# Performance work log

Measured on AMD Instinct MI355X. Metric: run time of the kernel, lower is better.

## Reference

```python
import jax, jax.numpy as jnp
import numpy as np

N_NODES = 50000
N_EDGES = 800000
F_IN = 1024
F_MID = 256
DROP_P = 0.5


def gcn_conv(x, W, b, src, dst, norm, n_nodes):
    # x: [N, Fin], W: [Fin, Fout]. PyG GCNConv: out = scatter(norm * (xW)[src] -> dst) + b
    h = x @ W                                  # [N, Fout]
    msg = h[src] * norm[:, None]               # [E+N, Fout] gathered, normalized messages
    out = jax.ops.segment_sum(msg, dst, num_segments=n_nodes)
    return out + b


def setup_inputs() -> dict:
    key = jax.random.key(0)
    k1, k2, k3, k4, k5 = jax.random.split(key, 5)
    x = jax.random.normal(k1, (N_NODES, F_IN), dtype=jnp.float32)
    edge_index = jax.random.randint(k2, (2, N_EDGES), 0, N_NODES, dtype=jnp.int64)
    # Glorot-ish init for GCN weights
    W1 = jax.random.normal(k3, (F_IN, F_MID), dtype=jnp.float32) / np.sqrt(F_IN)
    b1 = jnp.zeros((F_MID,), dtype=jnp.float32)
    W2 = jax.random.normal(k4, (F_MID, F_IN), dtype=jnp.float32) / np.sqrt(F_MID)
    b2 = jnp.zeros((F_IN,), dtype=jnp.float32)
    return {"x": x, "edge_index": edge_index, "W1": W1, "b1": b1, "W2": W2, "b2": b2}


def reference(x, edge_index, W1, b1, W2, b2):
    n = x.shape[0]
    # add self-loops (PyG GCNConv default add_self_loops=True)
    loop = jnp.arange(n, dtype=edge_index.dtype)
    src = jnp.concatenate([edge_index[0], loop])
    dst = jnp.concatenate([edge_index[1], loop])
    # symmetric normalization D^-1/2 (A+I) D^-1/2
    deg = jax.ops.segment_sum(jnp.ones_like(dst, dtype=x.dtype), dst, num_segments=n)
    dinv = jnp.where(deg > 0, jax.lax.rsqrt(deg), 0.0)
    norm = dinv[src] * dinv[dst]               # [E+N]

    h = jax.nn.relu(gcn_conv(x, W1, b1, src, dst, norm, n))
    # F.dropout(x) default: p=0.5, training=True -> deterministic mask w/ fixed key
    keep = jax.random.bernoulli(jax.random.key(42), 1.0 - DROP_P, h.shape)
    h = jnp.where(keep, h / (1.0 - DROP_P), 0.0)
    out = gcn_conv(h, W2, b2, src, dst, norm, n)
    return out
```

## Files before the change

### kernel.cpp

```cpp
#include <hip/hip_runtime.h>
#include <hip/hip_bf16.h>

#define N_NODES 50000
#define N_EDGES 800000
#define F_IN 1024
#define F_MID 256

typedef _Float16 f16;
typedef _Float16 f16x4 __attribute__((ext_vector_type(4)));
typedef _Float16 f16x8 __attribute__((ext_vector_type(8)));
typedef float f32x4 __attribute__((ext_vector_type(4)));

__device__ __forceinline__ void glds16(const f16* g, f16* l) {
    __builtin_amdgcn_global_load_lds(
        (const __attribute__((address_space(1))) unsigned int*)g,
        (__attribute__((address_space(3))) unsigned int*)l, 16, 0, 0);
}

__device__ __forceinline__ void tf_round(unsigned &x0, unsigned &x1, int r) {
    x0 += x1;
    x1 = (x1 << r) | (x1 >> (32 - r));
    x1 ^= x0;
}

__device__ __forceinline__ int keep_mask(unsigned f) {
    const unsigned ks0 = 0u, ks1 = 42u;
    const unsigned ks2 = ks0 ^ ks1 ^ 0x1BD11BDAu;
    unsigned x0 = 0u + ks0;
    unsigned x1 = f + ks1;
    tf_round(x0,x1,13); tf_round(x0,x1,15); tf_round(x0,x1,26); tf_round(x0,x1,6);
    x0 += ks1; x1 += ks2 + 1u;
    tf_round(x0,x1,17); tf_round(x0,x1,29); tf_round(x0,x1,16); tf_round(x0,x1,24);
    x0 += ks2; x1 += ks0 + 2u;
    tf_round(x0,x1,13); tf_round(x0,x1,15); tf_round(x0,x1,26); tf_round(x0,x1,6);
    x0 += ks0; x1 += ks1 + 3u;
    tf_round(x0,x1,17); tf_round(x0,x1,29); tf_round(x0,x1,16); tf_round(x0,x1,24);
    x0 += ks1; x1 += ks2 + 4u;
    tf_round(x0,x1,13); tf_round(x0,x1,15); tf_round(x0,x1,26); tf_round(x0,x1,6);
    x0 += ks2; x1 += ks0 + 5u;
    return (((x0 ^ x1) >> 31) == 0u);
}

__device__ __forceinline__ int ld_src(const int* ei, int e, int is64) {
    return is64 ? ei[2 * e] : ei[e];
}
__device__ __forceinline__ int ld_dst(const int* ei, int e, int is64) {
    return is64 ? ei[2 * N_EDGES + 2 * e] : ei[N_EDGES + e];
}

__global__ __launch_bounds__(256) void k_prep(const float* __restrict__ W1, f16* __restrict__ W1T,
                                              const int* __restrict__ ei,
                                              int* deg, int* cursor, int* counter, int* flag) {
    const int tid = threadIdx.x;
    const int gid = blockIdx.x * 256 + tid;
    const int gstr = gridDim.x * 256;
    if (gid < N_NODES) { deg[gid] = 0; cursor[gid] = 0; }
    if (gid == 0) counter[0] = 0;
    if (blockIdx.x == 0) {
        if (tid == 0) flag[0] = 1;
        __syncthreads();
        int nz = 0;
        for (int k = tid; k < 1024; k += 256) nz |= (ei[2 * k + 1] != 0);
        if (nz) atomicAnd(flag, 0);
    }
    for (int i = gid; i < F_IN * F_MID; i += gstr) {
        int k = i >> 8, n = i & 255;
        W1T[(size_t)n * F_IN + (k ^ ((n & 7) << 3))] = (f16)W1[i];
    }
}

__global__ __launch_bounds__(256) void k_rows(const int* __restrict__ deg, float* __restrict__ dinv,
                                              int* __restrict__ rowst, int* __restrict__ counter) {
    int i = blockIdx.x * 256 + threadIdx.x;
    if (i < N_NODES) {
        dinv[i] = rsqrtf((float)(deg[i] + 1));
        rowst[i] = atomicAdd(counter, deg[i]);
    }
}

__global__ __launch_bounds__(256) void k_fill(const int* __restrict__ ei, const int* __restrict__ rowst,
                                              int* __restrict__ cursor, int* __restrict__ csr,
                                              const int* __restrict__ flag) {
    int e = blockIdx.x * 256 + threadIdx.x;
    int is64 = flag[0];
    if (e < N_EDGES) {
        int d = ld_dst(ei, e, is64);
        int pos = rowst[d] + atomicAdd(&cursor[d], 1);
        csr[pos] = ld_src(ei, e, is64);
    }
}

template<int BM, int BN, int TN, bool A16, bool C16>
__global__ __launch_bounds__(TN) void k_mfma(const void* __restrict__ Ag,
                                             const f16* __restrict__ BTg,
                                             void* __restrict__ Cg,
                                             const float* __restrict__ bias,
                                             int M, int Ntot, int K, int mainx,
                                             const int* __restrict__ ei, int* __restrict__ deg,
                                             const int* __restrict__ flag,
                                             const float* __restrict__ Wr, f16* __restrict__ WrT) {
    if ((int)blockIdx.x >= mainx) {
        const int str = (gridDim.x - mainx) * TN;
        const int t0 = (blockIdx.x - mainx) * TN + threadIdx.x;
        const int is64 = flag[0];
        for (int e = t0; e < N_EDGES; e += str)
            atomicAdd(&deg[ld_dst(ei, e, is64)], 1);
        for (int i = t0; i < F_MID * F_IN; i += str) {
            int k = i >> 10, n = i & 1023;
            WrT[(size_t)n * F_MID + (k ^ ((n & 7) << 3))] = (f16)Wr[i];
        }
        return;
    }

    constexpr int BK = 64;
    constexpr int NW = TN / 64;
    constexpr int WM = BM / 64;
    constexpr int WN = NW / WM;
    constexpr int WTN = BN / WN;
    constexpr int FN = WTN / 16;
    __shared__ f16 As[2][BM * BK];
    __shared__ f16 Bs[2][BN * BK];

    const int tid = threadIdx.x, lane = tid & 63, wid = tid >> 6;
    const int wm = wid % WM, wn = wid / WM;
    const int row0 = blockIdx.x * BM, col0 = blockIdx.y * BN;

    f32x4 acc[4][FN] = {};
    const int ar = tid >> 3;
    const int ac = (tid & 7) * 8;
    f32x4 av0 = {}, av1 = {};

    const int nkt = K / BK;
    int buf = 0;

    auto stage_load = [&](int kt, int b) {
        const int k0 = kt * BK;
        if constexpr (A16) {
            const f16* A = (const f16*)Ag;
            constexpr int nA = BM / 8 / NW;
            #pragma unroll
            for (int j = 0; j < nA; ++j) {
                int i = wid * nA + j;
                int li = i * 512 + lane * 8;
                int r = li >> 6, c = li & 63;
                glds16(&A[(size_t)(row0 + r) * K + k0 + c], &As[b][i * 512]);
            }
        } else {
            const float* A = (const float*)Ag;
            int gr = row0 + ar;
            if (gr < M) {
                av0 = *(const f32x4*)&A[(size_t)gr * K + k0 + ac];
                av1 = *(const f32x4*)&A[(size_t)gr * K + k0 + ac + 4];
            } else { av0 = (f32x4){}; av1 = (f32x4){}; }
        }
        constexpr int nB = BN / 8 / NW;
        #pragma unroll
        for (int j = 0; j < nB; ++j) {
            int i = wid * nB + j;
            int li = i * 512 + lane * 8;
            int r = li >> 6, c = li & 63;
            glds16(&BTg[(size_t)(col0 + r) * K + k0 + c], &Bs[b][i * 512]);
        }
    };
    auto stage_write = [&](int b) {
        if constexpr (!A16) {
            f16x4 l = __builtin_convertvector(av0, f16x4);
            f16x4 h = __builtin_convertvector(av1, f16x4);
            f16x8 v = { l[0], l[1], l[2], l[3], h[0], h[1], h[2], h[3] };
            *(f16x8*)&As[b][ar * 64 + (ac ^ ((ar & 7) << 3))] = v;
        }
    };

    stage_load(0, 0);
    stage_write(0);
    __syncthreads();

    for (int kt = 0; kt < nkt; ++kt) {
        if (kt + 1 < nkt) stage_load(kt + 1, buf ^ 1);
        #pragma unroll
        for (int ks = 0; ks < 2; ++ks) {
            const int cc = ks * 32 + (lane >> 4) * 8;
            f16x8 af[4], bf[FN];
            #pragma unroll
            for (int m = 0; m < 4; ++m) {
                int r = wm * 64 + m * 16 + (lane & 15);
                af[m] = *(const f16x8*)&As[buf][r * 64 + (cc ^ ((r & 7) << 3))];
            }
            #pragma unroll
            for (int n = 0; n < FN; ++n) {
                int r = wn * WTN + n * 16 + (lane & 15);
                bf[n] = *(const f16x8*)&Bs[buf][r * 64 + (cc ^ ((r & 7) << 3))];
            }
            #pragma unroll
            for (int m = 0; m < 4; ++m)
                #pragma unroll
                for (int n = 0; n < FN; ++n)
                    acc[m][n] = __builtin_amdgcn_mfma_f32_16x16x32_f16(af[m], bf[n], acc[m][n], 0, 0, 0);
        }
        if (kt + 1 < nkt) stage_write(buf ^ 1);
        __syncthreads();
        buf ^= 1;
    }

    const int rbase = row0 + wm * 64 + (lane >> 4) * 4;
    const int cbase = col0 + wn * WTN + (lane & 15);
    #pragma unroll
    for (int m = 0; m < 4; ++m) {
        #pragma unroll
        for (int j = 0; j < 4; ++j) {
            const int r = rbase + m * 16 + j;
            if (r >= M) continue;
            if constexpr (C16) {
                f16* C = (f16*)Cg;
                #pragma unroll
                for (int n = 0; n < FN; ++n)
                    C[(size_t)r * Ntot + cbase + n * 16] = (f16)acc[m][n][j];
            } else {
                float* C = (float*)Cg;
                #pragma unroll
                for (int n = 0; n < FN; ++n) {
                    const int c = cbase + n * 16;
                    C[(size_t)r * Ntot + c] = acc[m][n][j] + bias[c];
                }
            }
        }
    }
}

template<int POST, int SWZ, int SCALED_IN>
__global__ __launch_bounds__(256) void k_agg16(const f16* __restrict__ hin,
                                               f16* __restrict__ hout,
                                               const int* __restrict__ csr,
                                               const int* __restrict__ rowst,
                                               const int* __restrict__ deg,
                                               const float* __restrict__ dinv,
                                               const float* __restrict__ bias) {
    const int wid = threadIdx.x >> 6;
    const int lane = threadIdx.x & 63;
    const int row = blockIdx.x * 4 + wid;
    const int start = rowst[row];
    const int cnt = deg[row];
    const int ch = lane * 4;
    const float di = dinv[row];

    f32x4 acc = __builtin_convertvector(*(const f16x4*)&hin[(size_t)row * F_MID + ch], f32x4);
    if (!SCALED_IN) acc *= di;
    int k = 0;
    for (; k + 4 <= cnt; k += 4) {
        const int s0 = csr[start + k], s1 = csr[start + k + 1];
        const int s2 = csr[start + k + 2], s3 = csr[start + k + 3];
        f16x4 v0 = *(const f16x4*)&hin[(size_t)s0 * F_MID + ch];
        f16x4 v1 = *(const f16x4*)&hin[(size_t)s1 * F_MID + ch];
        f16x4 v2 = *(const f16x4*)&hin[(size_t)s2 * F_MID + ch];
        f16x4 v3 = *(const f16x4*)&hin[(size_t)s3 * F_MID + ch];
        if (SCALED_IN) {
            acc += __builtin_convertvector(v0, f32x4) + __builtin_convertvector(v1, f32x4)
                 + __builtin_convertvector(v2, f32x4) + __builtin_convertvector(v3, f32x4);
        } else {
            acc += dinv[s0] * __builtin_convertvector(v0, f32x4)
                 + dinv[s1] * __builtin_convertvector(v1, f32x4)
                 + dinv[s2] * __builtin_convertvector(v2, f32x4)
                 + dinv[s3] * __builtin_convertvector(v3, f32x4);
        }
    }
    for (; k < cnt; ++k) {
        const int s = csr[start + k];
        f32x4 v = __builtin_convertvector(*(const f16x4*)&hin[(size_t)s * F_MID + ch], f32x4);
        acc += SCALED_IN ? v : dinv[s] * v;
    }
    acc *= di;

    if (POST) {
        const unsigned f0 = (unsigned)row * F_MID + (unsigned)ch;
        #pragma unroll
        for (int j = 0; j < 4; ++j) {
            float t = acc[j] + bias[ch + j];
            t = fmaxf(t, 0.0f);
            t = keep_mask(f0 + j) ? t * 2.0f : 0.0f;
            acc[j] = t * di;
        }
    }
    const int oc = SWZ ? (ch ^ ((row & 7) << 3)) : ch;
    *(f16x4*)&hout[(size_t)row * F_MID + oc] = __builtin_convertvector(acc, f16x4);
}

extern "C" void kernel_launch(void* const* d_in, const int* in_sizes, int n_in,
                              void* d_out, int out_size, void* d_ws, size_t ws_size,
                              hipStream_t stream) {
    const float* x  = (const float*)d_in[0];
    const int*   ei = (const int*)d_in[1];
    const float* W1 = (const float*)d_in[2];
    const float* b1 = (const float*)d_in[3];
    const float* W2 = (const float*)d_in[4];
    const float* b2 = (const float*)d_in[5];
    float* out = (float*)d_out;

    f16* h0 = (f16*)out;
    f16* h1s = h0 + (size_t)N_NODES * F_MID;

    f16*   h2agg = (f16*)d_ws;
    f16*   W1T   = h2agg + (size_t)(N_NODES + 64) * F_MID;
    f16*   W2T   = W1T + (size_t)F_MID * F_IN;
    float* dinv  = (float*)(W2T + (size_t)F_IN * F_MID);
    int*   deg   = (int*)(dinv + N_NODES);
    int*   rowst = deg + N_NODES;
    int*   cursor= rowst + N_NODES;
    int*   csr   = cursor + N_NODES;
    int*   counter = csr + N_EDGES;
    int*   flag    = counter + 1;

    k_prep<<<256, 256, 0, stream>>>(W1, W1T, ei, deg, cursor, counter, flag);

    {
        const int mainx = (N_NODES + 63) / 64;
        dim3 grid(mainx + 384, 1);
        k_mfma<64, 256, 512, false, true><<<grid, 512, 0, stream>>>(
            (const void*)x, W1T, (void*)h0, nullptr, N_NODES, F_MID, F_IN,
            mainx, ei, deg, flag, W2, W2T);
    }

    k_rows<<<(N_NODES + 255) / 256, 256, 0, stream>>>(deg, dinv, rowst, counter);
    k_fill<<<(N_EDGES + 255) / 256, 256, 0, stream>>>(ei, rowst, cursor, csr, flag);

    k_agg16<1, 0, 0><<<N_NODES / 4, 256, 0, stream>>>(h0, h1s, csr, rowst, deg, dinv, b1);
    k_agg16<0, 1, 1><<<N_NODES / 4, 256, 0, stream>>>(h1s, h2agg, csr, rowst, deg, dinv, nullptr);

    {
        const int mainx = (N_NODES + 63) / 64;
        dim3 grid(mainx, 4);
        k_mfma<64, 256, 512, true, false><<<grid, 512, 0, stream>>>(
            (const void*)h2agg, W2T, (void*)out, b2, N_NODES, F_IN, F_MID,
            mainx, ei, deg, flag, W2, W2T);
    }
}
```

Measured before the change: 349.9 us.

## Stage GEMM epilogue through LDS for vectorized coalesced stores, add nontemporal loads

The MFMA GEMM epilogue now writes accumulators into a shared-memory tile, which aliases the staging buffers, and then emits 16-byte coalesced global stores. Previously it did scattered scalar stores per lane. Fp32 input loads and the final output stores become nontemporal, and the number of auxiliary prep blocks launched alongside the first GEMM drops. The aim is to cut store transaction count and cache pollution, at the cost of an extra barrier and LDS round-trip in the epilogue.

```diff
diff --git a/kernel.cpp b/kernel.cpp
--- a/kernel.cpp
+++ b/kernel.cpp
@@ -118,10 +118,16 @@
     constexpr int WN = NW / WM;
     constexpr int WTN = BN / WN;
     constexpr int FN = WTN / 16;
-    __shared__ f16 As[2][BM * BK];
-    __shared__ f16 Bs[2][BN * BK];
+    constexpr int SMEM_STG = (2 * BM * BK + 2 * BN * BK) * 2;
+    constexpr int LDC = BN + 8;
+    constexpr int SMEM_EPI = BM * LDC * (C16 ? 2 : 4);
+    constexpr int SMEM_SZ = SMEM_STG > SMEM_EPI ? SMEM_STG : SMEM_EPI;
+    __shared__ __align__(16) char smem[SMEM_SZ];
+    f16* As_ = (f16*)smem;
+    f16* Bs_ = As_ + 2 * BM * BK;
 
     const int tid = threadIdx.x, lane = tid & 63, wid = tid >> 6;
+    const int l15 = lane & 15;
     const int wm = wid % WM, wn = wid / WM;
     const int row0 = blockIdx.x * BM, col0 = blockIdx.y * BN;
 
@@ -137,29 +143,25 @@
         const int k0 = kt * BK;
         if constexpr (A16) {
             const f16* A = (const f16*)Ag;
-            constexpr int nA = BM / 8 / NW;
-            #pragma unroll
-            for (int j = 0; j < nA; ++j) {
-                int i = wid * nA + j;
+            #pragma unroll
+            for (int i = wid; i < BM * BK / 512; i += NW) {
                 int li = i * 512 + lane * 8;
                 int r = li >> 6, c = li & 63;
-                glds16(&A[(size_t)(row0 + r) * K + k0 + c], &As[b][i * 512]);
+                glds16(&A[(size_t)(row0 + r) * K + k0 + c], &As_[b * BM * BK + i * 512]);
             }
         } else {
             const float* A = (const float*)Ag;
             int gr = row0 + ar;
             if (gr < M) {
-                av0 = *(const f32x4*)&A[(size_t)gr * K + k0 + ac];
-                av1 = *(const f32x4*)&A[(size_t)gr * K + k0 + ac + 4];
+                av0 = __builtin_nontemporal_load((const f32x4*)&A[(size_t)gr * K + k0 + ac]);
+                av1 = __builtin_nontemporal_load((const f32x4*)&A[(size_t)gr * K + k0 + ac + 4]);
             } else { av0 = (f32x4){}; av1 = (f32x4){}; }
         }
-        constexpr int nB = BN / 8 / NW;
-        #pragma unroll
-        for (int j = 0; j < nB; ++j) {
-            int i = wid * nB + j;
+        #pragma unroll
+        for (int i = wid; i < BN * BK / 512; i += NW) {
             int li = i * 512 + lane * 8;
             int r = li >> 6, c = li & 63;
-            glds16(&BTg[(size_t)(col0 + r) * K + k0 + c], &Bs[b][i * 512]);
+            glds16(&BTg[(size_t)(col0 + r) * K + k0 + c], &Bs_[b * BN * BK + i * 512]);
         }
     };
     auto stage_write = [&](int b) {
@@ -167,7 +169,7 @@
             f16x4 l = __builtin_convertvector(av0, f16x4);
             f16x4 h = __builtin_convertvector(av1, f16x4);
             f16x8 v = { l[0], l[1], l[2], l[3], h[0], h[1], h[2], h[3] };
-            *(f16x8*)&As[b][ar * 64 + (ac ^ ((ar & 7) << 3))] = v;
+            *(f16x8*)&As_[b * BM * BK + ar * 64 + (ac ^ ((ar & 7) << 3))] = v;
         }
     };
 
@@ -183,13 +185,13 @@
             f16x8 af[4], bf[FN];
             #pragma unroll
             for (int m = 0; m < 4; ++m) {
-                int r = wm * 64 + m * 16 + (lane & 15);
-                af[m] = *(const f16x8*)&As[buf][r * 64 + (cc ^ ((r & 7) << 3))];
+                int r = wm * 64 + m * 16 + l15;
+                af[m] = *(const f16x8*)&As_[buf * BM * BK + r * 64 + (cc ^ ((r & 7) << 3))];
             }
             #pragma unroll
             for (int n = 0; n < FN; ++n) {
-                int r = wn * WTN + n * 16 + (lane & 15);
-                bf[n] = *(const f16x8*)&Bs[buf][r * 64 + (cc ^ ((r & 7) << 3))];
+                int r = wn * WTN + n * 16 + l15;
+                bf[n] = *(const f16x8*)&Bs_[buf * BN * BK + r * 64 + (cc ^ ((r & 7) << 3))];
             }
             #pragma unroll
             for (int m = 0; m < 4; ++m)
@@ -202,26 +204,51 @@
         buf ^= 1;
     }
 
-    const int rbase = row0 + wm * 64 + (lane >> 4) * 4;
-    const int cbase = col0 + wn * WTN + (lane & 15);
-    #pragma unroll
-    for (int m = 0; m < 4; ++m) {
-        #pragma unroll
-        for (int j = 0; j < 4; ++j) {
-            const int r = rbase + m * 16 + j;
-            if (r >= M) continue;
-            if constexpr (C16) {
-                f16* C = (f16*)Cg;
+    if constexpr (C16) {
+        f16* CT = (f16*)smem;
+        #pragma unroll
+        for (int m = 0; m < 4; ++m)
+            #pragma unroll
+            for (int j = 0; j < 4; ++j) {
+                const int rl = wm * 64 + m * 16 + (lane >> 4) * 4 + j;
                 #pragma unroll
                 for (int n = 0; n < FN; ++n)
-                    C[(size_t)r * Ntot + cbase + n * 16] = (f16)acc[m][n][j];
-            } else {
-                float* C = (float*)Cg;
+                    CT[rl * LDC + wn * WTN + n * 16 + l15] = (f16)acc[m][n][j];
+            }
+        __syncthreads();
+        f16* C = (f16*)Cg;
+        constexpr int NCH = BM * BN / 8;
+        #pragma unroll
+        for (int ci = tid; ci < NCH; ci += TN) {
+            const int r = ci / (BN / 8), c = (ci % (BN / 8)) * 8;
+            const int gr = row0 + r;
+            if (gr < M) {
+                f16x8 v = *(const f16x8*)&CT[r * LDC + c];
+                *(f16x8*)&C[(size_t)gr * Ntot + col0 + c] = v;
+            }
+        }
+    } else {
+        float* CT = (float*)smem;
+        #pragma unroll
+        for (int m = 0; m < 4; ++m)
+            #pragma unroll
+            for (int j = 0; j < 4; ++j) {
+                const int rl = wm * 64 + m * 16 + (lane >> 4) * 4 + j;
                 #pragma unroll
-                for (int n = 0; n < FN; ++n) {
-                    const int c = cbase + n * 16;
-                    C[(size_t)r * Ntot + c] = acc[m][n][j] + bias[c];
-                }
+                for (int n = 0; n < FN; ++n)
+                    CT[rl * LDC + wn * WTN + n * 16 + l15] = acc[m][n][j];
+            }
+        __syncthreads();
+        float* C = (float*)Cg;
+        constexpr int NCH = BM * BN / 4;
+        #pragma unroll
+        for (int ci = tid; ci < NCH; ci += TN) {
+            const int r = ci / (BN / 4), c = (ci % (BN / 4)) * 4;
+            const int gr = row0 + r;
+            if (gr < M) {
+                f32x4 v = *(const f32x4*)&CT[r * LDC + c];
+                v += *(const f32x4*)&bias[col0 + c];
+                __builtin_nontemporal_store(v, (f32x4*)&C[(size_t)gr * Ntot + col0 + c]);
             }
         }
     }
@@ -313,7 +340,7 @@
 
     {
         const int mainx = (N_NODES + 63) / 64;
-        dim3 grid(mainx + 384, 1);
+        dim3 grid(mainx + 240, 1);
         k_mfma<64, 256, 512, false, true><<<grid, 512, 0, stream>>>(
             (const void*)x, W1T, (void*)h0, nullptr, N_NODES, F_MID, F_IN,
             mainx, ei, deg, flag, W2, W2T);
```

Result: no change. 344.2 us, median of 3 (-1.6%).
